# Kernel optimization log

Hardware: AMD Instinct MI355X
Metric: run time of the kernel (lower is better)

The kernel has to match this reference:

```python
import jax, jax.numpy as jnp
import numpy as np

V = 49688; D = 128; Hd = 256; DM = 2 * Hd; FF = 4 * Hd; NH = 4
B = 256; O = 32; L = 32

def _ln(x, g, b, eps=1e-5):
    m = x.mean(-1, keepdims=True)
    v = x.var(-1, keepdims=True)
    return (x - m) / jnp.sqrt(v + eps) * g + b

def _mha(x, in_w, in_b, out_w, out_b, nh):
    Bx, S, E = x.shape
    hd = E // nh
    qkv = x @ in_w.T + in_b
    q, k, v = jnp.split(qkv, 3, axis=-1)
    sp = lambda t: t.reshape(Bx, S, nh, hd).transpose(0, 2, 1, 3)
    q, k, v = sp(q), sp(k), sp(v)
    s = jnp.einsum('bhqd,bhkd->bhqk', q, k) / jnp.sqrt(jnp.asarray(hd, x.dtype))
    o = jnp.einsum('bhqk,bhkd->bhqd', jax.nn.softmax(s, -1), v)
    o = o.transpose(0, 2, 1, 3).reshape(Bx, S, E)
    return o @ out_w.T + out_b

def _gru_dir(x, wih, whh, bih, bhh):
    Bx, T, _ = x.shape
    H = whh.shape[1]
    def step(h, xt):
        gi = xt @ wih.T + bih
        gh = h @ whh.T + bhh
        ir, iz, inn = jnp.split(gi, 3, -1)
        hr, hz, hn = jnp.split(gh, 3, -1)
        r = jax.nn.sigmoid(ir + hr)
        z = jax.nn.sigmoid(iz + hz)
        n = jnp.tanh(inn + r * hn)
        h = (1 - z) * n + z * h
        return h, h
    _, hs = jax.lax.scan(step, jnp.zeros((Bx, H), x.dtype), jnp.swapaxes(x, 0, 1))
    return jnp.swapaxes(hs, 0, 1)

def setup_inputs():
    key = jax.random.key(0)
    it = iter(jax.random.split(key, 48))
    def nrm(shape, s=0.05):
        return jax.random.normal(next(it), shape, jnp.float32) * s
    inp = {}
    inp['order_history'] = jax.random.randint(next(it), (B, O, L), 0, V + 1)
    inp['days_between'] = jax.random.uniform(next(it), (B, O - 1), jnp.float32) * 30.0
    inp['days_since_last'] = jax.random.uniform(next(it), (B,), jnp.float32) * 30.0
    inp['emb'] = nrm((V + 1, D), 1.0).at[0].set(0.0)  # padding_idx=0 -> zero row
    inp['a_in_w'] = nrm((3 * D, D)); inp['a_in_b'] = jnp.zeros((3 * D,))
    inp['a_out_w'] = nrm((D, D)); inp['a_out_b'] = jnp.zeros((D,))
    for d in ('f', 'b'):
        inp['g_wih_' + d] = nrm((3 * Hd, D)); inp['g_whh_' + d] = nrm((3 * Hd, Hd))
        inp['g_bih_' + d] = jnp.zeros((3 * Hd,)); inp['g_bhh_' + d] = jnp.zeros((3 * Hd,))
    inp['t_in_w'] = nrm((3 * DM, DM)); inp['t_in_b'] = jnp.zeros((3 * DM,))
    inp['t_out_w'] = nrm((DM, DM)); inp['t_out_b'] = jnp.zeros((DM,))
    inp['t_ln1_g'] = jnp.ones((DM,)); inp['t_ln1_b'] = jnp.zeros((DM,))
    inp['t_ff1_w'] = nrm((FF, DM)); inp['t_ff1_b'] = jnp.zeros((FF,))
    inp['t_ff2_w'] = nrm((DM, FF)); inp['t_ff2_b'] = jnp.zeros((DM,))
    inp['t_ln2_g'] = jnp.ones((DM,)); inp['t_ln2_b'] = jnp.zeros((DM,))
    inp['te1_w'] = nrm((Hd // 4, 2)); inp['te1_b'] = jnp.zeros((Hd // 4,))
    inp['te_ln1_g'] = jnp.ones((Hd // 4,)); inp['te_ln1_b'] = jnp.zeros((Hd // 4,))
    inp['te2_w'] = nrm((Hd // 2, Hd // 4)); inp['te2_b'] = jnp.zeros((Hd // 2,))
    inp['te_ln2_g'] = jnp.ones((Hd // 2,)); inp['te_ln2_b'] = jnp.zeros((Hd // 2,))
    inp['c_w'] = nrm((Hd, 2 * Hd + Hd // 2)); inp['c_b'] = jnp.zeros((Hd,))
    inp['c_ln_g'] = jnp.ones((Hd,)); inp['c_ln_b'] = jnp.zeros((Hd,))
    return inp

def reference(order_history, days_between, days_since_last, emb, a_in_w, a_in_b, a_out_w, a_out_b, g_wih_f, g_whh_f, g_bih_f, g_bhh_f, g_wih_b, g_whh_b, g_bih_b, g_bhh_b, t_in_w, t_in_b, t_out_w, t_out_b, t_ln1_g, t_ln1_b, t_ff1_w, t_ff1_b, t_ff2_w, t_ff2_b, t_ln2_g, t_ln2_b, te1_w, te1_b, te_ln1_g, te_ln1_b, te2_w, te2_b, te_ln2_g, te_ln2_b, c_w, c_b, c_ln_g, c_ln_b):
    Bx, Ox, Lx = order_history.shape
    # per-order item self-attention, batched over all (user, order) pairs
    x = emb[order_history].reshape(Bx * Ox, Lx, -1)                  # [B*O, L, D]
    x = _mha(x, a_in_w, a_in_b, a_out_w, a_out_b, NH)
    order_emb = x.mean(1).reshape(Bx, Ox, -1)                        # [B, O, D]
    # bidirectional GRU over the order sequence
    hf = _gru_dir(order_emb, g_wih_f, g_whh_f, g_bih_f, g_bhh_f)
    hb = _gru_dir(order_emb[:, ::-1], g_wih_b, g_whh_b, g_bih_b, g_bhh_b)[:, ::-1]
    g = jnp.concatenate([hf, hb], -1)                                # [B, O, 2H]
    # post-LN TransformerEncoderLayer (relu, dropout in eval mode)
    a = _mha(g, t_in_w, t_in_b, t_out_w, t_out_b, NH)
    g = _ln(g + a, t_ln1_g, t_ln1_b)
    f = jax.nn.relu(g @ t_ff1_w.T + t_ff1_b) @ t_ff2_w.T + t_ff2_b
    g = _ln(g + f, t_ln2_g, t_ln2_b)
    enc = g.mean(1)                                                  # [B, 2H]
    # temporal features: only days_mean and recency are used (std computed but unused in original)
    feats = jnp.stack([days_between.mean(1), days_since_last], 1)    # [B, 2]
    te = jax.nn.relu(_ln(feats @ te1_w.T + te1_b, te_ln1_g, te_ln1_b))
    te = jax.nn.relu(_ln(te @ te2_w.T + te2_b, te_ln2_g, te_ln2_b))  # [B, H/2]
    out = jax.nn.relu(_ln(jnp.concatenate([enc, te], 1) @ c_w.T + c_b, c_ln_g, c_ln_b))
    return out                                                       # [B, H]
```

## Files before the change

kernel.cpp:

```cpp
#include <hip/hip_runtime.h>
#include <hip/hip_bf16.h>
#include <math.h>

typedef __hip_bfloat16 bf16;
typedef __attribute__((ext_vector_type(8))) short short8v;
typedef __attribute__((ext_vector_type(4))) short short4v;
typedef __attribute__((ext_vector_type(4))) float float4v;
#define MFMA16 __builtin_amdgcn_mfma_f32_16x16x32_bf16

__device__ __forceinline__ float us2f(unsigned short u) {
  union { unsigned u; float f; } c; c.u = ((unsigned)u) << 16; return c.f;
}
__device__ __forceinline__ unsigned short f2us(float f) {
  return __bfloat16_as_ushort(__float2bfloat16(f));
}

__device__ __forceinline__ float dot_ff(const float* __restrict__ x,
                                        const float* __restrict__ w, int K) {
  const float4* xp = reinterpret_cast<const float4*>(x);
  const float4* wp = reinterpret_cast<const float4*>(w);
  float acc = 0.f;
  const int n = K >> 2;
  for (int i = 0; i < n; ++i) {
    float4 a = xp[i], b = wp[i];
    acc += a.x*b.x + a.y*b.y + a.z*b.z + a.w*b.w;
  }
  return acc;
}

__device__ __forceinline__ float sigm(float x) { return 1.f / (1.f + __expf(-x)); }
__device__ __forceinline__ float tanh_fast(float x) {
  x = fminf(fmaxf(x, -15.f), 15.f);
  float e = __expf(2.f * x);
  return (e - 1.f) / (e + 1.f);
}

__global__ void k_canary(float* __restrict__ out) {
  out[blockIdx.x * 256 + threadIdx.x] = 100.0f;
}

__global__ __launch_bounds__(256) void k_cvt(
    const float* __restrict__ a_in_w, const float* __restrict__ t_in_w,
    const float* __restrict__ t_out_w, const float* __restrict__ t_ff1w,
    const float* __restrict__ t_ff2w, const float* __restrict__ a_out_w,
    unsigned short* __restrict__ awb, unsigned short* __restrict__ twb,
    unsigned short* __restrict__ pwb, unsigned short* __restrict__ f1wb,
    unsigned short* __restrict__ f2wb, unsigned short* __restrict__ awb2)
{
  int i = blockIdx.x * 256 + threadIdx.x;
  if (i < 49152)  awb[i] = f2us(a_in_w[i]);
  if (i < 786432) twb[i] = f2us(t_in_w[i]);
  if (i < 262144) pwb[i] = f2us(t_out_w[i]);
  if (i < 524288) f1wb[i] = f2us(t_ff1w[i]);
  if (i < 524288) f2wb[i] = f2us(t_ff2w[i]);
  if (i < 16384)  awb2[i] = f2us(a_out_w[i]);
}

__global__ __launch_bounds__(256) void k_gru_wb(
    const float* __restrict__ wih_f, const float* __restrict__ whh_f,
    const float* __restrict__ wih_b, const float* __restrict__ whh_b,
    unsigned short* __restrict__ whhb, unsigned short* __restrict__ wihb)
{
  int i = blockIdx.x * 256 + threadIdx.x;
  if (i >= 393216) return;
  int dir = i / 196608, r = i % 196608;
  whhb[i] = f2us((dir ? whh_b : whh_f)[r]);
  if (r < 98304) wihb[dir * 98304 + r] = f2us((dir ? wih_b : wih_f)[r]);
}

__global__ __launch_bounds__(256, 2) void k_qkvpre(
    const float* __restrict__ emb, const unsigned short* __restrict__ awb,
    const float* __restrict__ in_b,
    unsigned short* __restrict__ qkt, unsigned short* __restrict__ vt)
{
  const int row0 = blockIdx.x * 32, tid = threadIdx.x;
  __shared__ alignas(16) unsigned short xs[32 * 136];
  for (int i = tid; i < 1024; i += 256) {
    int t = i >> 5, c4 = (i & 31) << 2;
    int grow = row0 + t; if (grow > 49688) grow = 49688;
    float4 e4 = *reinterpret_cast<const float4*>(emb + (size_t)grow * 128 + c4);
    short4v s; s[0] = f2us(e4.x); s[1] = f2us(e4.y); s[2] = f2us(e4.z); s[3] = f2us(e4.w);
    *reinterpret_cast<short4v*>(xs + t * 136 + c4) = s;
  }
  __syncthreads();
  const int lane = tid & 63, wave = tid >> 6;
  const int l15 = lane & 15, quad = lane >> 4;
  short8v af[2][4];
#pragma unroll
  for (int mt = 0; mt < 2; ++mt)
#pragma unroll
    for (int kc = 0; kc < 4; ++kc)
      af[mt][kc] = *reinterpret_cast<const short8v*>(
          xs + (mt * 16 + l15) * 136 + kc * 32 + quad * 8);
  for (int ni = 0; ni < 6; ++ni) {
    const int j = (wave + ni * 4) * 16 + l15;
    const unsigned short* wrow = awb + (size_t)j * 128;
    float4v acc0 = {0.f, 0.f, 0.f, 0.f}, acc1 = {0.f, 0.f, 0.f, 0.f};
#pragma unroll
    for (int kc = 0; kc < 4; ++kc) {
      short8v bfr = *reinterpret_cast<const short8v*>(wrow + kc * 32 + quad * 8);
      acc0 = MFMA16(af[0][kc], bfr, acc0, 0, 0, 0);
      acc1 = MFMA16(af[1][kc], bfr, acc1, 0, 0, 0);
    }
    const float bj = in_b[j];
#pragma unroll
    for (int r = 0; r < 4; ++r) {
      int g0 = row0 + quad * 4 + r, g1 = g0 + 16;
      if (j < 256) {
        if (g0 <= 49688) qkt[(size_t)g0 * 256 + j] = f2us(acc0[r] + bj);
        if (g1 <= 49688) qkt[(size_t)g1 * 256 + j] = f2us(acc1[r] + bj);
      } else {
        int jj = j - 256;
        if (g0 <= 49688) vt[(size_t)g0 * 128 + jj] = f2us(acc0[r] + bj);
        if (g1 <= 49688) vt[(size_t)g1 * 128 + jj] = f2us(acc1[r] + bj);
      }
    }
  }
}

__global__ __launch_bounds__(256, 5) void k_order_attn(
    const int* __restrict__ oh, const unsigned short* __restrict__ qkt,
    const unsigned short* __restrict__ vt,
    const unsigned short* __restrict__ awb2, const float* __restrict__ out_b,
    unsigned short* __restrict__ oeb)
{
  const int bo = blockIdx.x;
  const int tid = threadIdx.x;
  __shared__ alignas(16) unsigned short qb[32 * 136];
  __shared__ alignas(16) unsigned short kb[32 * 136];
  __shared__ alignas(16) unsigned short vTb[128 * 32];
  unsigned short* ob = qb;
  unsigned short* pb = kb;

  const int lane = tid & 63, wave = tid >> 6;
  const int l15 = lane & 15, quad = lane >> 4;

  for (int i = tid; i < 1024; i += 256) {
    int t = i >> 5, c8 = (i & 31) << 3;
    int id = oh[bo * 32 + t];
    short8v v8 = *reinterpret_cast<const short8v*>(qkt + (size_t)id * 256 + c8);
    if (c8 < 128) *reinterpret_cast<short8v*>(qb + t * 136 + c8) = v8;
    else          *reinterpret_cast<short8v*>(kb + t * 136 + (c8 - 128)) = v8;
  }
  for (int i = tid; i < 512; i += 256) {
    int t = i >> 4, c8 = (i & 15) << 3;
    int id = oh[bo * 32 + t];
    short8v v8 = *reinterpret_cast<const short8v*>(vt + (size_t)id * 128 + c8);
#pragma unroll
    for (int j2 = 0; j2 < 8; ++j2) vTb[(c8 + j2) * 32 + t] = v8[j2];
  }
  __syncthreads();
  {
    const int h = wave;
    const float scale1 = 0.17677669529663687f;
    short8v qf[2], kf[2];
#pragma unroll
    for (int mt = 0; mt < 2; ++mt)
      qf[mt] = *reinterpret_cast<const short8v*>(qb + (mt * 16 + l15) * 136 + h * 32 + quad * 8);
#pragma unroll
    for (int nt = 0; nt < 2; ++nt)
      kf[nt] = *reinterpret_cast<const short8v*>(kb + (nt * 16 + l15) * 136 + h * 32 + quad * 8);
    float4v sacc[2][2];
#pragma unroll
    for (int mt = 0; mt < 2; ++mt)
#pragma unroll
      for (int nt = 0; nt < 2; ++nt) {
        sacc[mt][nt] = (float4v){0.f, 0.f, 0.f, 0.f};
        sacc[mt][nt] = MFMA16(qf[mt], kf[nt], sacc[mt][nt], 0, 0, 0);
      }
    __syncthreads();
#pragma unroll
    for (int mt = 0; mt < 2; ++mt)
#pragma unroll
      for (int r = 0; r < 4; ++r) {
        float e0 = __expf(sacc[mt][0][r] * scale1);
        float e1 = __expf(sacc[mt][1][r] * scale1);
        int row = h * 32 + mt * 16 + quad * 4 + r;
        pb[row * 32 + l15] = f2us(e0);
        pb[row * 32 + 16 + l15] = f2us(e1);
      }
    short8v ones;
#pragma unroll
    for (int i = 0; i < 8; ++i) ones[i] = (short)0x3F80;
    short8v pf[2], vf[2];
#pragma unroll
    for (int mt = 0; mt < 2; ++mt)
      pf[mt] = *reinterpret_cast<const short8v*>(pb + (h * 32 + mt * 16 + l15) * 32 + quad * 8);
    float4v sums[2];
#pragma unroll
    for (int mt = 0; mt < 2; ++mt) {
      sums[mt] = (float4v){0.f, 0.f, 0.f, 0.f};
      sums[mt] = MFMA16(pf[mt], ones, sums[mt], 0, 0, 0);
    }
#pragma unroll
    for (int nt = 0; nt < 2; ++nt)
      vf[nt] = *reinterpret_cast<const short8v*>(vTb + (h * 32 + nt * 16 + l15) * 32 + quad * 8);
    float4v oacc[2][2];
#pragma unroll
    for (int mt = 0; mt < 2; ++mt)
#pragma unroll
      for (int nt = 0; nt < 2; ++nt) {
        oacc[mt][nt] = (float4v){0.f, 0.f, 0.f, 0.f};
        oacc[mt][nt] = MFMA16(pf[mt], vf[nt], oacc[mt][nt], 0, 0, 0);
      }
#pragma unroll
    for (int mt = 0; mt < 2; ++mt)
#pragma unroll
      for (int r = 0; r < 4; ++r) {
        int t = mt * 16 + quad * 4 + r;
        float inv = 1.f / sums[mt][r];
#pragma unroll
        for (int nt = 0; nt < 2; ++nt)
          ob[t * 136 + h * 32 + nt * 16 + l15] = f2us(oacc[mt][nt][r] * inv);
      }
  }
  __syncthreads();
  {
    float4v acc[2][2];
#pragma unroll
    for (int mt = 0; mt < 2; ++mt)
#pragma unroll
      for (int nt = 0; nt < 2; ++nt) acc[mt][nt] = (float4v){0.f, 0.f, 0.f, 0.f};
#pragma unroll
    for (int kc = 0; kc < 4; ++kc) {
      short8v af0 = *reinterpret_cast<const short8v*>(ob + l15 * 136 + kc * 32 + quad * 8);
      short8v af1 = *reinterpret_cast<const short8v*>(ob + (16 + l15) * 136 + kc * 32 + quad * 8);
#pragma unroll
      for (int nt = 0; nt < 2; ++nt) {
        int j = (wave * 2 + nt) * 16 + l15;
        short8v bfr = *reinterpret_cast<const short8v*>(awb2 + (size_t)j * 128 + kc * 32 + quad * 8);
        acc[0][nt] = MFMA16(af0, bfr, acc[0][nt], 0, 0, 0);
        acc[1][nt] = MFMA16(af1, bfr, acc[1][nt], 0, 0, 0);
      }
    }
#pragma unroll
    for (int nt = 0; nt < 2; ++nt) {
      float part = 0.f;
#pragma unroll
      for (int mt = 0; mt < 2; ++mt)
#pragma unroll
        for (int r = 0; r < 4; ++r) part += acc[mt][nt][r];
      part += __shfl_xor(part, 16);
      part += __shfl_xor(part, 32);
      if (quad == 0) {
        int j = (wave * 2 + nt) * 16 + l15;
        oeb[(size_t)bo * 128 + j] = f2us(part * (1.f / 32.f) + out_b[j]);
      }
    }
  }
}

__global__ __launch_bounds__(256, 2) void k_gru_gi(
    const unsigned short* __restrict__ oeb, const unsigned short* __restrict__ wihb,
    unsigned short* __restrict__ gi)
{
  const int row0 = blockIdx.x * 32, tid = threadIdx.x;
  __shared__ alignas(16) unsigned short xs[32 * 136];
  for (int i = tid; i < 512; i += 256) {
    int t = i >> 4, c8 = (i & 15) << 3;
    *reinterpret_cast<short8v*>(xs + t * 136 + c8) =
        *reinterpret_cast<const short8v*>(oeb + (size_t)(row0 + t) * 128 + c8);
  }
  __syncthreads();
  const int lane = tid & 63, wave = tid >> 6;
  const int l15 = lane & 15, quad = lane >> 4;
  short8v af[2][4];
#pragma unroll
  for (int mt = 0; mt < 2; ++mt)
#pragma unroll
    for (int kc = 0; kc < 4; ++kc)
      af[mt][kc] = *reinterpret_cast<const short8v*>(
          xs + (mt * 16 + l15) * 136 + kc * 32 + quad * 8);
  for (int ni = 0; ni < 24; ++ni) {
    int col = (wave + ni * 4) * 16 + l15;
    const unsigned short* wrow = wihb + (size_t)col * 128;
    float4v a0 = {0.f,0.f,0.f,0.f}, a1 = {0.f,0.f,0.f,0.f};
#pragma unroll
    for (int kc = 0; kc < 4; ++kc) {
      short8v bfr = *reinterpret_cast<const short8v*>(wrow + kc * 32 + quad * 8);
      a0 = MFMA16(af[0][kc], bfr, a0, 0, 0, 0);
      a1 = MFMA16(af[1][kc], bfr, a1, 0, 0, 0);
    }
#pragma unroll
    for (int r = 0; r < 4; ++r) {
      gi[(size_t)(row0 + quad * 4 + r) * 1536 + col] = f2us(a0[r]);
      gi[(size_t)(row0 + quad * 4 + r + 16) * 1536 + col] = f2us(a1[r]);
    }
  }
}

__global__ __launch_bounds__(512, 2) void k_gru_rec(
    const unsigned short* __restrict__ gi, const unsigned short* __restrict__ whhb,
    const float* __restrict__ bih_f, const float* __restrict__ bhh_f,
    const float* __restrict__ bih_b, const float* __restrict__ bhh_b,
    float* __restrict__ g)
{
  const int b0 = blockIdx.x * 2, dir = blockIdx.y;
  const int tid = threadIdx.x;
  const unsigned short* wb = whhb + (size_t)dir * 196608;
  const float* bih = dir ? bih_b : bih_f;
  const float* bhh = dir ? bhh_b : bhh_f;
  __shared__ alignas(16) unsigned short hb[16 * 264];
  __shared__ float pg[2 * 772];
  const int lane = tid & 63, wave = tid >> 6;
  const int l15 = lane & 15, quad = lane >> 4;
  const int j = tid & 255, mb = tid >> 8;
  const float bir = bih[j], biz = bih[256 + j], bin_ = bih[512 + j];
  const float bhr = bhh[j], bhz = bhh[256 + j], bhn  = bhh[512 + j];
  short8v wf[6][8];
  int cols[6];
#pragma unroll
  for (int ni = 0; ni < 6; ++ni) {
    cols[ni] = (wave + ni * 8) * 16 + l15;
#pragma unroll
    for (int kc = 0; kc < 8; ++kc)
      wf[ni][kc] = *reinterpret_cast<const short8v*>(
          wb + (size_t)cols[ni] * 256 + kc * 32 + quad * 8);
  }
  for (int i = tid; i < 16 * 264; i += 512) hb[i] = 0;
  int tcur = dir ? 31 : 0;
  size_t gbase = ((size_t)(b0 + mb) * 32 + tcur) * 1536 + dir * 768;
  float gr = us2f(gi[gbase + j]);
  float gz = us2f(gi[gbase + 256 + j]);
  float gn = us2f(gi[gbase + 512 + j]);
  __syncthreads();
  for (int s = 0; s < 32; ++s) {
    float4v acc[6];
#pragma unroll
    for (int ni = 0; ni < 6; ++ni) acc[ni] = (float4v){0.f, 0.f, 0.f, 0.f};
#pragma unroll
    for (int kc = 0; kc < 8; ++kc) {
      short8v af = *reinterpret_cast<const short8v*>(hb + l15 * 264 + kc * 32 + quad * 8);
#pragma unroll
      for (int ni = 0; ni < 6; ++ni)
        acc[ni] = MFMA16(af, wf[ni][kc], acc[ni], 0, 0, 0);
    }
    if (quad == 0) {
#pragma unroll
      for (int ni = 0; ni < 6; ++ni) {
        pg[cols[ni]] = acc[ni][0];
        pg[772 + cols[ni]] = acc[ni][1];
      }
    }
    float gr2 = 0.f, gz2 = 0.f, gn2 = 0.f;
    if (s < 31) {
      int t2 = dir ? (30 - s) : (s + 1);
      size_t gb2 = ((size_t)(b0 + mb) * 32 + t2) * 1536 + dir * 768;
      gr2 = us2f(gi[gb2 + j]);
      gz2 = us2f(gi[gb2 + 256 + j]);
      gn2 = us2f(gi[gb2 + 512 + j]);
    }
    __syncthreads();
    {
      const int tt = dir ? (31 - s) : s;
      float hprev = us2f(hb[mb * 264 + j]);
      float r = sigm(gr + bir + pg[mb * 772 + j] + bhr);
      float z = sigm(gz + biz + pg[mb * 772 + 256 + j] + bhz);
      float n = tanh_fast(gn + bin_ + r * (pg[mb * 772 + 512 + j] + bhn));
      float nh = (1.f - z) * n + z * hprev;
      hb[mb * 264 + j] = f2us(nh);
      g[((size_t)(b0 + mb) * 32 + tt) * 512 + dir * 256 + j] = nh;
    }
    gr = gr2; gz = gz2; gn = gn2;
    __syncthreads();
  }
}

__global__ __launch_bounds__(256, 4) void k_mha2f(
    const float* __restrict__ g, const unsigned short* __restrict__ twb,
    const float* __restrict__ Bv, float* __restrict__ attn)
{
  const int b = blockIdx.x, h = blockIdx.y, tid = threadIdx.x;
  __shared__ alignas(16) unsigned short xs3[32 * 136];
  __shared__ alignas(16) unsigned short qk[2 * 32 * 136];
  __shared__ alignas(16) unsigned short vT[128 * 40];
  unsigned short* qs = qk;
  unsigned short* ks = qk + 32 * 136;
  unsigned short* pb = xs3;
  const int lane = tid & 63, wave = tid >> 6;
  const int l15 = lane & 15, quad = lane >> 4;

  int wrowi[6];
#pragma unroll
  for (int ni = 0; ni < 6; ++ni) {
    int idx = (wave + ni * 4) * 16 + l15;
    int m = idx >> 7, dd = idx & 127;
    wrowi[ni] = m * 512 + h * 128 + dd;
  }
  float4v acc[6][2];
#pragma unroll
  for (int ni = 0; ni < 6; ++ni)
#pragma unroll
    for (int mt = 0; mt < 2; ++mt) acc[ni][mt] = (float4v){0.f, 0.f, 0.f, 0.f};

  for (int ck = 0; ck < 4; ++ck) {
    __syncthreads();
    for (int i = tid; i < 1024; i += 256) {
      int t = i >> 5, c4 = (i & 31) << 2;
      float4 e4 = *reinterpret_cast<const float4*>(
          g + (size_t)b * 16384 + t * 512 + ck * 128 + c4);
      short4v s; s[0] = f2us(e4.x); s[1] = f2us(e4.y); s[2] = f2us(e4.z); s[3] = f2us(e4.w);
      *reinterpret_cast<short4v*>(xs3 + t * 136 + c4) = s;
    }
    __syncthreads();
    short8v af2[2][4];
#pragma unroll
    for (int mt = 0; mt < 2; ++mt)
#pragma unroll
      for (int u = 0; u < 4; ++u)
        af2[mt][u] = *reinterpret_cast<const short8v*>(
            xs3 + (mt * 16 + l15) * 136 + u * 32 + quad * 8);
#pragma unroll
    for (int ni = 0; ni < 6; ++ni) {
      const unsigned short* wrow = twb + (size_t)wrowi[ni] * 512 + ck * 128;
#pragma unroll
      for (int u = 0; u < 4; ++u) {
        short8v bfr = *reinterpret_cast<const short8v*>(wrow + u * 32 + quad * 8);
        acc[ni][0] = MFMA16(af2[0][u], bfr, acc[ni][0], 0, 0, 0);
        acc[ni][1] = MFMA16(af2[1][u], bfr, acc[ni][1], 0, 0, 0);
      }
    }
  }
  __syncthreads();
#pragma unroll
  for (int ni = 0; ni < 6; ++ni) {
    int idx = (wave + ni * 4) * 16 + l15;
    int m = idx >> 7, dd = idx & 127;
    float bj = Bv[wrowi[ni]];
    if (m < 2) {
      unsigned short* dst = (m == 0) ? qs : ks;
#pragma unroll
      for (int r = 0; r < 4; ++r) {
        int t0 = quad * 4 + r;
        dst[t0 * 136 + dd] = f2us(acc[ni][0][r] + bj);
        dst[(t0 + 16) * 136 + dd] = f2us(acc[ni][1][r] + bj);
      }
    } else {
      short4v s0, s1;
#pragma unroll
      for (int r = 0; r < 4; ++r) { s0[r] = f2us(acc[ni][0][r] + bj); s1[r] = f2us(acc[ni][1][r] + bj); }
      *reinterpret_cast<short4v*>(vT + dd * 40 + quad * 4) = s0;
      *reinterpret_cast<short4v*>(vT + dd * 40 + 16 + quad * 4) = s1;
    }
  }
  __syncthreads();
  {
    const float scale2 = 0.08838834764831845f;
    const int mt = wave >> 1, nt = wave & 1;
    float4v a = {0.f, 0.f, 0.f, 0.f};
#pragma unroll
    for (int kc = 0; kc < 4; ++kc) {
      short8v qf = *reinterpret_cast<const short8v*>(qs + (mt * 16 + l15) * 136 + kc * 32 + quad * 8);
      short8v kf = *reinterpret_cast<const short8v*>(ks + (nt * 16 + l15) * 136 + kc * 32 + quad * 8);
      a = MFMA16(qf, kf, a, 0, 0, 0);
    }
#pragma unroll
    for (int r = 0; r < 4; ++r) {
      int row = mt * 16 + quad * 4 + r;
      pb[row * 32 + nt * 16 + l15] = f2us(__expf(a[r] * scale2));
    }
  }
  __syncthreads();
  {
    short8v ones;
#pragma unroll
    for (int i = 0; i < 8; ++i) ones[i] = (short)0x3F80;
    short8v pf[2], vf[2];
#pragma unroll
    for (int mt = 0; mt < 2; ++mt)
      pf[mt] = *reinterpret_cast<const short8v*>(pb + (mt * 16 + l15) * 32 + quad * 8);
    float4v sums[2];
#pragma unroll
    for (int mt = 0; mt < 2; ++mt) {
      sums[mt] = (float4v){0.f, 0.f, 0.f, 0.f};
      sums[mt] = MFMA16(pf[mt], ones, sums[mt], 0, 0, 0);
    }
#pragma unroll
    for (int ntl = 0; ntl < 2; ++ntl)
      vf[ntl] = *reinterpret_cast<const short8v*>(vT + ((2 * wave + ntl) * 16 + l15) * 40 + quad * 8);
    float4v oacc[2][2];
#pragma unroll
    for (int mt = 0; mt < 2; ++mt)
#pragma unroll
      for (int ntl = 0; ntl < 2; ++ntl) {
        oacc[mt][ntl] = (float4v){0.f, 0.f, 0.f, 0.f};
        oacc[mt][ntl] = MFMA16(pf[mt], vf[ntl], oacc[mt][ntl], 0, 0, 0);
      }
#pragma unroll
    for (int mt = 0; mt < 2; ++mt)
#pragma unroll
      for (int r = 0; r < 4; ++r) {
        int q = mt * 16 + quad * 4 + r;
        float inv = 1.f / sums[mt][r];
#pragma unroll
        for (int ntl = 0; ntl < 2; ++ntl)
          attn[((size_t)b * 32 + q) * 512 + h * 128 + (2 * wave + ntl) * 16 + l15] =
              oacc[mt][ntl][r] * inv;
      }
  }
}

__global__ __launch_bounds__(512, 2) void k_projln_mfma(
    const float* __restrict__ X, const unsigned short* __restrict__ Wb,
    const float* __restrict__ bias, const float* __restrict__ res,
    const float* __restrict__ gam, const float* __restrict__ bet,
    float* __restrict__ Y)
{
  const int row0 = blockIdx.x * 16, tid = threadIdx.x;
  __shared__ alignas(16) unsigned short xs[16 * 520];
  __shared__ float ys[16 * 516];
  for (int i = tid; i < 16 * 512; i += 512) {
    int t = i >> 9, c = i & 511;
    xs[t * 520 + c] = f2us(X[(size_t)(row0 + t) * 512 + c]);
  }
  __syncthreads();
  {
    const int lane = tid & 63, wave = tid >> 6;
    const int l15 = lane & 15, quad = lane >> 4;
    short8v af[16];
#pragma unroll
    for (int kc = 0; kc < 16; ++kc)
      af[kc] = *reinterpret_cast<const short8v*>(xs + l15 * 520 + kc * 32 + quad * 8);
    short8v bufA[16], bufB[16];
    {
      const unsigned short* w0 = Wb + (size_t)((wave + 0 * 8) * 16 + l15) * 512;
#pragma unroll
      for (int kc = 0; kc < 16; ++kc)
        bufA[kc] = *reinterpret_cast<const short8v*>(w0 + kc * 32 + quad * 8);
    }
#pragma unroll
    for (int ni = 0; ni < 4; ++ni) {
      short8v* cur = (ni & 1) ? bufB : bufA;
      short8v* nxt = (ni & 1) ? bufA : bufB;
      if (ni < 3) {
        const unsigned short* wn = Wb + (size_t)((wave + (ni + 1) * 8) * 16 + l15) * 512;
#pragma unroll
        for (int kc = 0; kc < 16; ++kc)
          nxt[kc] = *reinterpret_cast<const short8v*>(wn + kc * 32 + quad * 8);
      }
      float4v acc = {0.f,0.f,0.f,0.f};
#pragma unroll
      for (int kc = 0; kc < 16; ++kc)
        acc = MFMA16(af[kc], cur[kc], acc, 0, 0, 0);
      int col = (wave + ni * 8) * 16 + l15;
      float bj = bias[col];
#pragma unroll
      for (int r = 0; r < 4; ++r)
        ys[(quad * 4 + r) * 516 + col] = acc[r] + bj;
    }
  }
  __syncthreads();
  for (int i = tid; i < 16 * 512; i += 512) {
    int t = i >> 9, c = i & 511;
    ys[t * 516 + c] += res[(size_t)(row0 + t) * 512 + c];
  }
  __syncthreads();
  {
    int row = tid >> 5, l32 = tid & 31;
    const float* yr = ys + row * 516;
    float part = 0.f;
#pragma unroll
    for (int k = 0; k < 16; ++k) part += yr[l32 + 32 * k];
#pragma unroll
    for (int off = 16; off; off >>= 1) part += __shfl_xor(part, off, 32);
    float mean = part * (1.f / 512.f);
    float var = 0.f;
#pragma unroll
    for (int k = 0; k < 16; ++k) { float d = yr[l32 + 32 * k] - mean; var += d * d; }
#pragma unroll
    for (int off = 16; off; off >>= 1) var += __shfl_xor(var, off, 32);
    float rs = rsqrtf(var * (1.f / 512.f) + 1e-5f);
    for (int k = 0; k < 16; ++k) {
      int c = l32 + 32 * k;
      Y[(size_t)(row0 + row) * 512 + c] = (yr[c] - mean) * rs * gam[c] + bet[c];
    }
  }
}

__global__ __launch_bounds__(512, 2) void k_ff(
    const float* __restrict__ X, const unsigned short* __restrict__ W1,
    const float* __restrict__ b1, const unsigned short* __restrict__ W2,
    const float* __restrict__ b2, float* __restrict__ yraw)
{
  const int row0 = blockIdx.x * 32, tid = threadIdx.x;
  __shared__ alignas(16) unsigned short xs[32 * 520];
  __shared__ alignas(16) unsigned short f1c[32 * 136];
  const int lane = tid & 63, wave = tid >> 6;
  const int l15 = lane & 15, quad = lane >> 4;
  for (int i = tid; i < 4096; i += 512) {
    int t = i >> 7, c4 = (i & 127) << 2;
    float4 e4 = *reinterpret_cast<const float4*>(X + (size_t)(row0 + t) * 512 + c4);
    short4v s; s[0] = f2us(e4.x); s[1] = f2us(e4.y); s[2] = f2us(e4.z); s[3] = f2us(e4.w);
    *reinterpret_cast<short4v*>(xs + t * 520 + c4) = s;
  }
  __syncthreads();
  float4v acc2[2][4];
#pragma unroll
  for (int mt = 0; mt < 2; ++mt)
#pragma unroll
    for (int ni = 0; ni < 4; ++ni) acc2[mt][ni] = (float4v){0.f,0.f,0.f,0.f};
  int cols2[4];
#pragma unroll
  for (int ni = 0; ni < 4; ++ni) cols2[ni] = (wave + ni * 8) * 16 + l15;

  for (int ck = 0; ck < 8; ++ck) {
    {
      const int col = ck * 128 + wave * 16 + l15;
      const unsigned short* wrow = W1 + (size_t)col * 512;
      float4v a0 = {0.f,0.f,0.f,0.f}, a1 = {0.f,0.f,0.f,0.f};
#pragma unroll
      for (int kc = 0; kc < 16; ++kc) {
        short8v b = *reinterpret_cast<const short8v*>(wrow + kc * 32 + quad * 8);
        short8v x0 = *reinterpret_cast<const short8v*>(xs + l15 * 520 + kc * 32 + quad * 8);
        short8v x1 = *reinterpret_cast<const short8v*>(xs + (16 + l15) * 520 + kc * 32 + quad * 8);
        a0 = MFMA16(x0, b, a0, 0, 0, 0);
        a1 = MFMA16(x1, b, a1, 0, 0, 0);
      }
      const float bj = b1[col];
      const int cl = wave * 16 + l15;
#pragma unroll
      for (int r = 0; r < 4; ++r) {
        f1c[(quad * 4 + r) * 136 + cl] = f2us(fmaxf(a0[r] + bj, 0.f));
        f1c[(16 + quad * 4 + r) * 136 + cl] = f2us(fmaxf(a1[r] + bj, 0.f));
      }
    }
    __syncthreads();
#pragma unroll
    for (int ni = 0; ni < 4; ++ni) {
      const unsigned short* wrow2 = W2 + (size_t)cols2[ni] * 1024 + ck * 128;
#pragma unroll
      for (int kc = 0; kc < 4; ++kc) {
        short8v b = *reinterpret_cast<const short8v*>(wrow2 + kc * 32 + quad * 8);
        short8v a0 = *reinterpret_cast<const short8v*>(f1c + l15 * 136 + kc * 32 + quad * 8);
        short8v a1 = *reinterpret_cast<const short8v*>(f1c + (16 + l15) * 136 + kc * 32 + quad * 8);
        acc2[0][ni] = MFMA16(a0, b, acc2[0][ni], 0, 0, 0);
        acc2[1][ni] = MFMA16(a1, b, acc2[1][ni], 0, 0, 0);
      }
    }
    __syncthreads();
  }
#pragma unroll
  for (int mt = 0; mt < 2; ++mt)
#pragma unroll
    for (int ni = 0; ni < 4; ++ni) {
      int col = cols2[ni];
      float bj = b2[col];
#pragma unroll
      for (int r = 0; r < 4; ++r)
        yraw[(size_t)(row0 + mt * 16 + quad * 4 + r) * 512 + col] = acc2[mt][ni][r] + bj;
    }
}

__global__ __launch_bounds__(256, 2) void k_resln(
    const float* __restrict__ yraw, const float* __restrict__ res,
    const float* __restrict__ gam, const float* __restrict__ bet,
    float* __restrict__ Y)
{
  const int row0 = blockIdx.x * 16, tid = threadIdx.x;
  __shared__ float ys[16 * 516];
  for (int i = tid; i < 16 * 512; i += 256) {
    int t = i >> 9, c = i & 511;
    ys[t * 516 + c] = yraw[(size_t)(row0 + t) * 512 + c] +
                      res[(size_t)(row0 + t) * 512 + c];
  }
  __syncthreads();
  {
    int row = tid >> 4, l16 = tid & 15;
    const float* yr = ys + row * 516;
    float part = 0.f;
#pragma unroll
    for (int k = 0; k < 32; ++k) part += yr[l16 + 16 * k];
#pragma unroll
    for (int off = 8; off; off >>= 1) part += __shfl_xor(part, off, 16);
    float mean = part * (1.f / 512.f);
    float var = 0.f;
#pragma unroll
    for (int k = 0; k < 32; ++k) { float d = yr[l16 + 16 * k] - mean; var += d * d; }
#pragma unroll
    for (int off = 8; off; off >>= 1) var += __shfl_xor(var, off, 16);
    float rs = rsqrtf(var * (1.f / 512.f) + 1e-5f);
    for (int k = 0; k < 32; ++k) {
      int c = l16 + 16 * k;
      Y[(size_t)(row0 + row) * 512 + c] = (yr[c] - mean) * rs * gam[c] + bet[c];
    }
  }
}

__global__ __launch_bounds__(256) void k_final(
    const float* __restrict__ g2,
    const float* __restrict__ db, const float* __restrict__ dsl,
    const float* __restrict__ te1_w, const float* __restrict__ te1_b,
    const float* __restrict__ l1g, const float* __restrict__ l1b,
    const float* __restrict__ te2_w, const float* __restrict__ te2_b,
    const float* __restrict__ l2g, const float* __restrict__ l2b,
    const float* __restrict__ c_w, const float* __restrict__ c_b,
    const float* __restrict__ clg, const float* __restrict__ clb,
    float* __restrict__ out)
{
  const int b = blockIdx.x, tid = threadIdx.x;
  __shared__ float cat[640];
  __shared__ float t1[64];
  __shared__ float t2[128];
  __shared__ float pre[256];
  __shared__ float red[256];
  __shared__ float st[2];
  for (int i = tid; i < 512; i += 256) {
    float acc = 0.f;
#pragma unroll
    for (int t = 0; t < 32; ++t) acc += g2[((size_t)b * 32 + t) * 512 + i];
    cat[i] = acc * (1.f / 32.f);
  }
  if (tid == 0) {
    float s = 0.f;
    for (int i = 0; i < 31; ++i) s += db[b * 31 + i];
    st[0] = s / 31.f;
    st[1] = dsl[b];
  }
  __syncthreads();
  const float f0 = st[0], f1v = st[1];
  if (tid < 64)
    t1[tid] = f0 * te1_w[tid * 2] + f1v * te1_w[tid * 2 + 1] + te1_b[tid];
  __syncthreads();
  if (tid == 0) {
    float m = 0.f; for (int i = 0; i < 64; ++i) m += t1[i]; m *= (1.f / 64.f);
    float v = 0.f; for (int i = 0; i < 64; ++i) { float d = t1[i] - m; v += d * d; }
    st[0] = m; st[1] = rsqrtf(v * (1.f / 64.f) + 1e-5f);
  }
  __syncthreads();
  if (tid < 64) {
    float v = (t1[tid] - st[0]) * st[1] * l1g[tid] + l1b[tid];
    t1[tid] = fmaxf(v, 0.f);
  }
  __syncthreads();
  if (tid < 128)
    t2[tid] = dot_ff(t1, te2_w + (size_t)tid * 64, 64) + te2_b[tid];
  __syncthreads();
  if (tid == 0) {
    float m = 0.f; for (int i = 0; i < 128; ++i) m += t2[i]; m *= (1.f / 128.f);
    float v = 0.f; for (int i = 0; i < 128; ++i) { float d = t2[i] - m; v += d * d; }
    st[0] = m; st[1] = rsqrtf(v * (1.f / 128.f) + 1e-5f);
  }
  __syncthreads();
  if (tid < 128) {
    float v = (t2[tid] - st[0]) * st[1] * l2g[tid] + l2b[tid];
    cat[512 + tid] = fmaxf(v, 0.f);
  }
  __syncthreads();
  pre[tid] = dot_ff(cat, c_w + (size_t)tid * 640, 640) + c_b[tid];
  red[tid] = pre[tid];
  __syncthreads();
  for (int s = 128; s > 0; s >>= 1) { if (tid < s) red[tid] += red[tid + s]; __syncthreads(); }
  const float m = red[0] * (1.f / 256.f);
  __syncthreads();
  const float d = pre[tid] - m;
  red[tid] = d * d;
  __syncthreads();
  for (int s = 128; s > 0; s >>= 1) { if (tid < s) red[tid] += red[tid + s]; __syncthreads(); }
  const float rs = rsqrtf(red[0] * (1.f / 256.f) + 1e-5f);
  float v = d * rs * clg[tid] + clb[tid];
  out[(size_t)b * 256 + tid] = fmaxf(v, 0.f);
}

extern "C" void kernel_launch(void* const* d_in, const int* in_sizes, int n_in,
                              void* d_out, int out_size, void* d_ws, size_t ws_size,
                              hipStream_t stream) {
  (void)in_sizes; (void)n_in; (void)out_size; (void)ws_size;
  const int*   oh     = (const int*)  d_in[0];
  const float* db     = (const float*)d_in[1];
  const float* dsl    = (const float*)d_in[2];
  const float* emb    = (const float*)d_in[3];
  const float* a_in_w = (const float*)d_in[4];
  const float* a_in_b = (const float*)d_in[5];
  const float* a_out_w= (const float*)d_in[6];
  const float* a_out_b= (const float*)d_in[7];
  const float* wih_f  = (const float*)d_in[8];
  const float* whh_f  = (const float*)d_in[9];
  const float* bih_f  = (const float*)d_in[10];
  const float* bhh_f  = (const float*)d_in[11];
  const float* wih_b  = (const float*)d_in[12];
  const float* whh_b  = (const float*)d_in[13];
  const float* bih_b  = (const float*)d_in[14];
  const float* bhh_b  = (const float*)d_in[15];
  const float* t_in_w = (const float*)d_in[16];
  const float* t_in_b = (const float*)d_in[17];
  const float* t_out_w= (const float*)d_in[18];
  const float* t_out_b= (const float*)d_in[19];
  const float* t_ln1g = (const float*)d_in[20];
  const float* t_ln1b = (const float*)d_in[21];
  const float* t_ff1w = (const float*)d_in[22];
  const float* t_ff1b = (const float*)d_in[23];
  const float* t_ff2w = (const float*)d_in[24];
  const float* t_ff2b = (const float*)d_in[25];
  const float* t_ln2g = (const float*)d_in[26];
  const float* t_ln2b = (const float*)d_in[27];
  const float* te1_w  = (const float*)d_in[28];
  const float* te1_b  = (const float*)d_in[29];
  const float* tl1g   = (const float*)d_in[30];
  const float* tl1b   = (const float*)d_in[31];
  const float* te2_w  = (const float*)d_in[32];
  const float* te2_b  = (const float*)d_in[33];
  const float* tl2g   = (const float*)d_in[34];
  const float* tl2b   = (const float*)d_in[35];
  const float* c_w    = (const float*)d_in[36];
  const float* c_b    = (const float*)d_in[37];
  const float* clng   = (const float*)d_in[38];
  const float* clnb   = (const float*)d_in[39];

  float* ws = (float*)d_ws;
  unsigned short* oeb  = (unsigned short*)ws;
  unsigned short* qkt  = (unsigned short*)(ws + 1048576);
  float* g    = ws + 1048576;
  float* yraw = ws + 1048576;
  float* attn = ws + 5242880;
  float* g1   = attn;
  float* g2   = attn;
  unsigned short* whhb = (unsigned short*)(ws + 9437184);
  unsigned short* wihb = (unsigned short*)(ws + 9633792);
  unsigned short* awb2 = (unsigned short*)(ws + 9732096);
  unsigned short* awb  = (unsigned short*)(ws + 10027008);
  unsigned short* twb  = (unsigned short*)(ws + 10051584);
  unsigned short* pwb  = (unsigned short*)(ws + 10444800);
  unsigned short* f1wb = (unsigned short*)(ws + 10575872);
  unsigned short* f2wb = (unsigned short*)(ws + 10838016);
  unsigned short* vt   = (unsigned short*)(ws + 11100160);
  unsigned short* gi   = (unsigned short*)(ws + 11100160);

  k_canary<<<256, 256, 0, stream>>>((float*)d_out);
  k_cvt<<<3072, 256, 0, stream>>>(a_in_w, t_in_w, t_out_w, t_ff1w, t_ff2w, a_out_w,
                                  awb, twb, pwb, f1wb, f2wb, awb2);
  k_gru_wb<<<1536, 256, 0, stream>>>(wih_f, whh_f, wih_b, whh_b, whhb, wihb);
  k_qkvpre<<<1553, 256, 0, stream>>>(emb, awb, a_in_b, qkt, vt);
  k_order_attn<<<8192, 256, 0, stream>>>(oh, qkt, vt, awb2, a_out_b, oeb);
  k_gru_gi<<<256, 256, 0, stream>>>(oeb, wihb, gi);
  k_gru_rec<<<dim3(128, 2), 512, 0, stream>>>(gi, whhb, bih_f, bhh_f, bih_b, bhh_b, g);
  k_mha2f<<<dim3(256, 4), 256, 0, stream>>>(g, twb, t_in_b, attn);
  k_projln_mfma<<<512, 512, 0, stream>>>(attn, pwb, t_out_b, g, t_ln1g, t_ln1b, g1);
  k_ff<<<256, 512, 0, stream>>>(g1, f1wb, t_ff1b, f2wb, t_ff2b, yraw);
  k_resln<<<512, 256, 0, stream>>>(yraw, g1, t_ln2g, t_ln2b, g2);
  k_final<<<256, 256, 0, stream>>>(g2, db, dsl, te1_w, te1_b, tl1g, tl1b,
                                   te2_w, te2_b, tl2g, tl2b, c_w, c_b, clng, clnb,
                                   (float*)d_out);
}
```

Measured before the change: 547.7 us.

## Split projection+LN into proj and resln kernels; widen FF blocks to 1024 threads

The fused attention-output-projection plus residual LayerNorm kernel is replaced by a plain projection kernel over 32-row tiles with 1024 threads, which writes raw fp32 output. The existing residual-LN kernel is then reused for LN1. The FF kernel moves to 1024 threads (16 waves), processing 256-wide hidden chunks in 4 iterations instead of 128-wide chunks in 8, which halves the barrier count. The gain is better weight reuse per block and fewer syncs, at the cost of an extra launch and a round trip of the projection output through global memory.

```diff
diff --git a/kernel.cpp b/kernel.cpp
--- a/kernel.cpp
+++ b/kernel.cpp
@@ -500,112 +500,72 @@
   }
 }
 
-__global__ __launch_bounds__(512, 2) void k_projln_mfma(
+__global__ __launch_bounds__(1024, 1) void k_proj(
     const float* __restrict__ X, const unsigned short* __restrict__ Wb,
-    const float* __restrict__ bias, const float* __restrict__ res,
-    const float* __restrict__ gam, const float* __restrict__ bet,
-    float* __restrict__ Y)
-{
-  const int row0 = blockIdx.x * 16, tid = threadIdx.x;
-  __shared__ alignas(16) unsigned short xs[16 * 520];
-  __shared__ float ys[16 * 516];
-  for (int i = tid; i < 16 * 512; i += 512) {
-    int t = i >> 9, c = i & 511;
-    xs[t * 520 + c] = f2us(X[(size_t)(row0 + t) * 512 + c]);
-  }
-  __syncthreads();
-  {
-    const int lane = tid & 63, wave = tid >> 6;
-    const int l15 = lane & 15, quad = lane >> 4;
-    short8v af[16];
-#pragma unroll
-    for (int kc = 0; kc < 16; ++kc)
-      af[kc] = *reinterpret_cast<const short8v*>(xs + l15 * 520 + kc * 32 + quad * 8);
-    short8v bufA[16], bufB[16];
-    {
-      const unsigned short* w0 = Wb + (size_t)((wave + 0 * 8) * 16 + l15) * 512;
-#pragma unroll
-      for (int kc = 0; kc < 16; ++kc)
-        bufA[kc] = *reinterpret_cast<const short8v*>(w0 + kc * 32 + quad * 8);
-    }
-#pragma unroll
-    for (int ni = 0; ni < 4; ++ni) {
-      short8v* cur = (ni & 1) ? bufB : bufA;
-      short8v* nxt = (ni & 1) ? bufA : bufB;
-      if (ni < 3) {
-        const unsigned short* wn = Wb + (size_t)((wave + (ni + 1) * 8) * 16 + l15) * 512;
-#pragma unroll
-        for (int kc = 0; kc < 16; ++kc)
-          nxt[kc] = *reinterpret_cast<const short8v*>(wn + kc * 32 + quad * 8);
-      }
-      float4v acc = {0.f,0.f,0.f,0.f};
-#pragma unroll
-      for (int kc = 0; kc < 16; ++kc)
-        acc = MFMA16(af[kc], cur[kc], acc, 0, 0, 0);
-      int col = (wave + ni * 8) * 16 + l15;
-      float bj = bias[col];
-#pragma unroll
-      for (int r = 0; r < 4; ++r)
-        ys[(quad * 4 + r) * 516 + col] = acc[r] + bj;
-    }
-  }
-  __syncthreads();
-  for (int i = tid; i < 16 * 512; i += 512) {
-    int t = i >> 9, c = i & 511;
-    ys[t * 516 + c] += res[(size_t)(row0 + t) * 512 + c];
-  }
-  __syncthreads();
-  {
-    int row = tid >> 5, l32 = tid & 31;
-    const float* yr = ys + row * 516;
-    float part = 0.f;
-#pragma unroll
-    for (int k = 0; k < 16; ++k) part += yr[l32 + 32 * k];
-#pragma unroll
-    for (int off = 16; off; off >>= 1) part += __shfl_xor(part, off, 32);
-    float mean = part * (1.f / 512.f);
-    float var = 0.f;
-#pragma unroll
-    for (int k = 0; k < 16; ++k) { float d = yr[l32 + 32 * k] - mean; var += d * d; }
-#pragma unroll
-    for (int off = 16; off; off >>= 1) var += __shfl_xor(var, off, 32);
-    float rs = rsqrtf(var * (1.f / 512.f) + 1e-5f);
-    for (int k = 0; k < 16; ++k) {
-      int c = l32 + 32 * k;
-      Y[(size_t)(row0 + row) * 512 + c] = (yr[c] - mean) * rs * gam[c] + bet[c];
-    }
-  }
-}
-
-__global__ __launch_bounds__(512, 2) void k_ff(
-    const float* __restrict__ X, const unsigned short* __restrict__ W1,
-    const float* __restrict__ b1, const unsigned short* __restrict__ W2,
-    const float* __restrict__ b2, float* __restrict__ yraw)
+    const float* __restrict__ bias, float* __restrict__ praw)
 {
   const int row0 = blockIdx.x * 32, tid = threadIdx.x;
   __shared__ alignas(16) unsigned short xs[32 * 520];
-  __shared__ alignas(16) unsigned short f1c[32 * 136];
   const int lane = tid & 63, wave = tid >> 6;
   const int l15 = lane & 15, quad = lane >> 4;
-  for (int i = tid; i < 4096; i += 512) {
+  for (int i = tid; i < 4096; i += 1024) {
     int t = i >> 7, c4 = (i & 127) << 2;
     float4 e4 = *reinterpret_cast<const float4*>(X + (size_t)(row0 + t) * 512 + c4);
     short4v s; s[0] = f2us(e4.x); s[1] = f2us(e4.y); s[2] = f2us(e4.z); s[3] = f2us(e4.w);
     *reinterpret_cast<short4v*>(xs + t * 520 + c4) = s;
   }
   __syncthreads();
-  float4v acc2[2][4];
+#pragma unroll
+  for (int ni = 0; ni < 2; ++ni) {
+    const int col = (wave + ni * 16) * 16 + l15;
+    const unsigned short* wrow = Wb + (size_t)col * 512;
+    float4v a0 = {0.f,0.f,0.f,0.f}, a1 = {0.f,0.f,0.f,0.f};
+#pragma unroll
+    for (int kc = 0; kc < 16; ++kc) {
+      short8v b = *reinterpret_cast<const short8v*>(wrow + kc * 32 + quad * 8);
+      short8v x0 = *reinterpret_cast<const short8v*>(xs + l15 * 520 + kc * 32 + quad * 8);
+      short8v x1 = *reinterpret_cast<const short8v*>(xs + (16 + l15) * 520 + kc * 32 + quad * 8);
+      a0 = MFMA16(x0, b, a0, 0, 0, 0);
+      a1 = MFMA16(x1, b, a1, 0, 0, 0);
+    }
+    const float bj = bias[col];
+#pragma unroll
+    for (int r = 0; r < 4; ++r) {
+      praw[(size_t)(row0 + quad * 4 + r) * 512 + col] = a0[r] + bj;
+      praw[(size_t)(row0 + 16 + quad * 4 + r) * 512 + col] = a1[r] + bj;
+    }
+  }
+}
+
+__global__ __launch_bounds__(1024, 1) void k_ff(
+    const float* __restrict__ X, const unsigned short* __restrict__ W1,
+    const float* __restrict__ b1, const unsigned short* __restrict__ W2,
+    const float* __restrict__ b2, float* __restrict__ yraw)
+{
+  const int row0 = blockIdx.x * 32, tid = threadIdx.x;
+  __shared__ alignas(16) unsigned short xs[32 * 520];
+  __shared__ alignas(16) unsigned short f1c[32 * 264];
+  const int lane = tid & 63, wave = tid >> 6;
+  const int l15 = lane & 15, quad = lane >> 4;
+  for (int i = tid; i < 4096; i += 1024) {
+    int t = i >> 7, c4 = (i & 127) << 2;
+    float4 e4 = *reinterpret_cast<const float4*>(X + (size_t)(row0 + t) * 512 + c4);
+    short4v s; s[0] = f2us(e4.x); s[1] = f2us(e4.y); s[2] = f2us(e4.z); s[3] = f2us(e4.w);
+    *reinterpret_cast<short4v*>(xs + t * 520 + c4) = s;
+  }
+  __syncthreads();
+  float4v acc2[2][2];
 #pragma unroll
   for (int mt = 0; mt < 2; ++mt)
 #pragma unroll
-    for (int ni = 0; ni < 4; ++ni) acc2[mt][ni] = (float4v){0.f,0.f,0.f,0.f};
-  int cols2[4];
-#pragma unroll
-  for (int ni = 0; ni < 4; ++ni) cols2[ni] = (wave + ni * 8) * 16 + l15;
-
-  for (int ck = 0; ck < 8; ++ck) {
+    for (int ni = 0; ni < 2; ++ni) acc2[mt][ni] = (float4v){0.f,0.f,0.f,0.f};
+  int cols2[2];
+#pragma unroll
+  for (int ni = 0; ni < 2; ++ni) cols2[ni] = (wave + ni * 16) * 16 + l15;
+
+  for (int ck = 0; ck < 4; ++ck) {
     {
-      const int col = ck * 128 + wave * 16 + l15;
+      const int col = ck * 256 + wave * 16 + l15;
       const unsigned short* wrow = W1 + (size_t)col * 512;
       float4v a0 = {0.f,0.f,0.f,0.f}, a1 = {0.f,0.f,0.f,0.f};
 #pragma unroll
@@ -620,19 +580,19 @@
       const int cl = wave * 16 + l15;
 #pragma unroll
       for (int r = 0; r < 4; ++r) {
-        f1c[(quad * 4 + r) * 136 + cl] = f2us(fmaxf(a0[r] + bj, 0.f));
-        f1c[(16 + quad * 4 + r) * 136 + cl] = f2us(fmaxf(a1[r] + bj, 0.f));
+        f1c[(quad * 4 + r) * 264 + cl] = f2us(fmaxf(a0[r] + bj, 0.f));
+        f1c[(16 + quad * 4 + r) * 264 + cl] = f2us(fmaxf(a1[r] + bj, 0.f));
       }
     }
     __syncthreads();
 #pragma unroll
-    for (int ni = 0; ni < 4; ++ni) {
-      const unsigned short* wrow2 = W2 + (size_t)cols2[ni] * 1024 + ck * 128;
-#pragma unroll
-      for (int kc = 0; kc < 4; ++kc) {
+    for (int ni = 0; ni < 2; ++ni) {
+      const unsigned short* wrow2 = W2 + (size_t)cols2[ni] * 1024 + ck * 256;
+#pragma unroll
+      for (int kc = 0; kc < 8; ++kc) {
         short8v b = *reinterpret_cast<const short8v*>(wrow2 + kc * 32 + quad * 8);
-        short8v a0 = *reinterpret_cast<const short8v*>(f1c + l15 * 136 + kc * 32 + quad * 8);
-        short8v a1 = *reinterpret_cast<const short8v*>(f1c + (16 + l15) * 136 + kc * 32 + quad * 8);
+        short8v a0 = *reinterpret_cast<const short8v*>(f1c + l15 * 264 + kc * 32 + quad * 8);
+        short8v a1 = *reinterpret_cast<const short8v*>(f1c + (16 + l15) * 264 + kc * 32 + quad * 8);
         acc2[0][ni] = MFMA16(a0, b, acc2[0][ni], 0, 0, 0);
         acc2[1][ni] = MFMA16(a1, b, acc2[1][ni], 0, 0, 0);
       }
@@ -642,7 +602,7 @@
 #pragma unroll
   for (int mt = 0; mt < 2; ++mt)
 #pragma unroll
-    for (int ni = 0; ni < 4; ++ni) {
+    for (int ni = 0; ni < 2; ++ni) {
       int col = cols2[ni];
       float bj = b2[col];
 #pragma unroll
@@ -824,6 +784,7 @@
   unsigned short* f2wb = (unsigned short*)(ws + 10838016);
   unsigned short* vt   = (unsigned short*)(ws + 11100160);
   unsigned short* gi   = (unsigned short*)(ws + 11100160);
+  float* praw = ws + 11100160;
 
   k_canary<<<256, 256, 0, stream>>>((float*)d_out);
   k_cvt<<<3072, 256, 0, stream>>>(a_in_w, t_in_w, t_out_w, t_ff1w, t_ff2w, a_out_w,
@@ -834,8 +795,9 @@
   k_gru_gi<<<256, 256, 0, stream>>>(oeb, wihb, gi);
   k_gru_rec<<<dim3(128, 2), 512, 0, stream>>>(gi, whhb, bih_f, bhh_f, bih_b, bhh_b, g);
   k_mha2f<<<dim3(256, 4), 256, 0, stream>>>(g, twb, t_in_b, attn);
-  k_projln_mfma<<<512, 512, 0, stream>>>(attn, pwb, t_out_b, g, t_ln1g, t_ln1b, g1);
-  k_ff<<<256, 512, 0, stream>>>(g1, f1wb, t_ff1b, f2wb, t_ff2b, yraw);
+  k_proj<<<256, 1024, 0, stream>>>(attn, pwb, t_out_b, praw);
+  k_resln<<<512, 256, 0, stream>>>(praw, g, t_ln1g, t_ln1b, g1);
+  k_ff<<<256, 1024, 0, stream>>>(g1, f1wb, t_ff1b, f2wb, t_ff2b, yraw);
   k_resln<<<512, 256, 0, stream>>>(yraw, g1, t_ln2g, t_ln2b, g2);
   k_final<<<256, 256, 0, stream>>>(g2, db, dsl, te1_w, te1_b, tl1g, tl1b,
                                    te2_w, te2_b, tl2g, tl2b, c_w, c_b, clng, clnb,
```

After: 526.3 us. 3.9% less time.
